# Optimization experiments

Hardware: AMD Instinct MI355X
Metric: run time of the kernel (lower is better)

Reference implementation:

```python
import math
import jax, jax.numpy as jnp
import numpy as np

SQ = 2048   # sequence length (hard-coded in source views)
B = 1       # batch (input_[:, 0, :] in QKVLinear)
H = 2048    # HIDDEN_SIZE
NH = 16     # NUM_HEADS
HD = 128    # head dim


def setup_inputs() -> dict:
    key = jax.random.key(0)
    ks = jax.random.split(key, 8)
    hidden_states = jax.random.normal(ks[0], (SQ, B, H), dtype=jnp.float32)
    # causal mask: True = masked (upper triangle, strictly above diagonal)
    attention_mask = jnp.triu(jnp.ones((SQ, SQ), dtype=bool), k=1)[None, None]
    qkv_w = jax.random.normal(ks[1], (3 * H, H), dtype=jnp.float32) * 0.02
    qkv_b = jax.random.normal(ks[2], (3 * H,), dtype=jnp.float32) * 0.02
    # SVD rotation matrices (approximately norm-preserving random matrices)
    svd_token = jax.random.normal(ks[3], (H, H), dtype=jnp.float32) / math.sqrt(H)
    svd_qk = jax.random.normal(ks[4], (NH, HD, HD), dtype=jnp.float32) / math.sqrt(HD)
    svd_vlin = jax.random.normal(ks[5], (NH, HD, HD), dtype=jnp.float32) / math.sqrt(HD)
    dense_w = jax.random.normal(ks[6], (NH, HD, H), dtype=jnp.float32) * 0.02
    dense_b = jax.random.normal(ks[7], (H,), dtype=jnp.float32) * 0.02
    return {
        "hidden_states": hidden_states,
        "attention_mask": attention_mask,
        "qkv_w": qkv_w,
        "qkv_b": qkv_b,
        "svd_token": svd_token,
        "svd_qk": svd_qk,
        "svd_vlin": svd_vlin,
        "dense_w": dense_w,
        "dense_b": dense_b,
    }


def reference(hidden_states, attention_mask, qkv_w, qkv_b, svd_token,
              svd_qk, svd_vlin, dense_w, dense_b):
    # QKVLinear: project input and weight through token-SVD (drop fraction = 0 -> no zeroing)
    x = hidden_states[:, 0, :] @ svd_token                 # [sq, H]
    w = qkv_w @ svd_token                                  # [3H, H]
    mixed = x @ w.T + qkv_b                                # [sq, 3H]
    mixed = mixed.reshape(SQ, B, NH, 3 * HD)
    q, k, v = jnp.split(mixed, 3, axis=-1)                 # each [sq, b, nh, hd]

    # per-head SVD-rotated Q/K (qk_drop = 0 -> h_mask is all-False, no zeroing)
    q = jnp.einsum('sbhd,hde->sbhe', q, svd_qk)
    k = jnp.einsum('sbhd,hde->sbhe', k, svd_qk)

    # scores: baddbmm with alpha = 1/(sqrt(hd)*coeff), then softmax rescales by coeff;
    # with layer_num=1 coeff=1, masked positions end at exactly -10000.
    scale = 1.0 / math.sqrt(HD)
    scores = jnp.einsum('sbhd,tbhd->bhst', q, k) * scale   # [b, nh, sq, sq]
    scores = jnp.where(attention_mask, -10000.0, scores)
    probs = jax.nn.softmax(scores, axis=-1)                # dropout in eval mode (identity)

    # per-head SVD-rotated V (vlinear_drop = 0 -> no zeroing)
    vv = jnp.einsum('sbhd,hde->sbhe', v, svd_vlin)
    ctx = jnp.einsum('bhst,tbhe->sbhe', probs, vv).reshape(SQ, B, H)

    # AttnOutputLinear: tsr block for head h = (dense_w[h].T @ svd_vlin[h]).T = svd_vlin[h].T @ dense_w[h]
    tsr = jnp.einsum('hde,hdo->heo', svd_vlin, dense_w).reshape(H, H)
    out = ctx @ tsr + dense_b                              # [sq, b, H]
    return out
```

## Files before the change

kernel.cpp:

```cpp
#include <hip/hip_runtime.h>
#include <hip/hip_bf16.h>
#include <stdint.h>
#include <math.h>


typedef __bf16 bf16_t;
typedef __bf16 bf16x8 __attribute__((ext_vector_type(8)));
typedef __bf16 bf16x4 __attribute__((ext_vector_type(4)));
typedef float  f32x4  __attribute__((ext_vector_type(4)));

__device__ __forceinline__ void async16(const void* g, void* l) {
  __builtin_amdgcn_global_load_lds(
      (const __attribute__((address_space(1))) void*)(uintptr_t)g,
      (__attribute__((address_space(3))) void*)(uint32_t)(uintptr_t)l,
      16, 0, 0);
}

#define FK_WAIT8() do { asm volatile("s_waitcnt vmcnt(8)" ::: "memory"); \
                        __builtin_amdgcn_sched_barrier(0); } while (0)
#define FK_WAIT4() do { asm volatile("s_waitcnt vmcnt(4)" ::: "memory"); \
                        __builtin_amdgcn_sched_barrier(0); } while (0)
#define FK_WAIT0() do { asm volatile("s_waitcnt vmcnt(0)" ::: "memory"); \
                        __builtin_amdgcn_sched_barrier(0); } while (0)
#define FK_BAR()   do { __builtin_amdgcn_s_barrier(); \
                        __builtin_amdgcn_sched_barrier(0); } while (0)

__device__ __forceinline__ void stage_half8(const bf16_t* __restrict__ P, int ld,
                                            int row0, int k0, bf16_t* lds,
                                            int w, int l)
{
  #pragma unroll
  for (int h = 0; h < 2; ++h) {
    const int r = h * 64 + w * 8 + (l >> 3);
    const int c = (l & 7) ^ (l >> 3);
    async16(P + (long long)(row0 + r) * ld + k0 + c * 8,
            lds + h * 4096 + w * 512);
  }
}

#define G8_READ_A(IH)                                                          \
  { _Pragma("unroll") for (int ii = 0; ii < 4; ++ii) {                         \
      _Pragma("unroll") for (int ks = 0; ks < 2; ++ks) {                       \
        const int rr = wmB + (IH) * 64 + ii * 16 + fr;                         \
        af[ii][ks] = *(const bf16x8*)&cA[rr * 64 + (((ks * 4 + kc) ^ (rr & 7)) * 8)]; \
      } } }

#define G8_READ_B(JH)                                                          \
  { _Pragma("unroll") for (int jj = 0; jj < 2; ++jj) {                         \
      _Pragma("unroll") for (int ks = 0; ks < 2; ++ks) {                       \
        const int rr = wnB + (JH) * 32 + jj * 16 + fr;                         \
        bfv[jj][ks] = *(const bf16x8*)&cB[rr * 64 + (((ks * 4 + kc) ^ (rr & 7)) * 8)]; \
      } } }

#define G8_MFMA(IH, JH)                                                        \
  { __builtin_amdgcn_s_setprio(1);                                             \
    _Pragma("unroll") for (int ks = 0; ks < 2; ++ks) {                         \
      _Pragma("unroll") for (int ii = 0; ii < 4; ++ii) {                       \
        _Pragma("unroll") for (int jj = 0; jj < 2; ++jj) {                     \
          acc[(IH) * 4 + ii][(JH) * 2 + jj] =                                  \
            __builtin_amdgcn_mfma_f32_16x16x32_bf16(af[ii][ks], bfv[jj][ks],   \
                acc[(IH) * 4 + ii][(JH) * 2 + jj], 0, 0, 0);                   \
        } } }                                                                  \
    __builtin_amdgcn_s_setprio(0); }

__global__ __launch_bounds__(512, 2)
void gemm8p(const bf16_t* __restrict__ A, const bf16_t* __restrict__ B,
            bf16_t* __restrict__ C, const bf16_t* __restrict__ bias,
            int K, int lda, int ldb, int ldc, int nbx)
{
  const int nwg = (int)gridDim.x;
  const int id  = (int)blockIdx.x;
  const int cpx = nwg >> 3;
  const int swz = (id & 7) * cpx + (id >> 3);
  const int by  = swz / nbx;
  const int bx  = swz - by * nbx;
  const int bm0 = by * 256;
  const int bn0 = bx * 256;

  __shared__ bf16_t sA[2][16384];
  __shared__ bf16_t sB[2][16384];

  const int t  = threadIdx.x;
  const int w  = t >> 6;
  const int l  = t & 63;
  const int fr = l & 15;
  const int kc = l >> 4;
  const int wmB = (w >> 2) * 128;
  const int wnB = (w & 3) * 64;

  float bvv[2][2];
  #pragma unroll
  for (int JH = 0; JH < 2; ++JH)
    #pragma unroll
    for (int jj = 0; jj < 2; ++jj)
      bvv[JH][jj] = (float)bias[bn0 + wnB + JH * 32 + jj * 16 + fr];

  f32x4 acc[8][4];
  #pragma unroll
  for (int i = 0; i < 8; ++i)
    #pragma unroll
    for (int j = 0; j < 4; ++j)
      #pragma unroll
      for (int r = 0; r < 4; ++r) acc[i][j][r] = 0.0f;

  const int nk = K >> 6;

  stage_half8(A, lda, bm0,       0, &sA[0][0],    w, l);
  stage_half8(A, lda, bm0 + 128, 0, &sA[0][8192], w, l);
  stage_half8(B, ldb, bn0,       0, &sB[0][0],    w, l);
  stage_half8(B, ldb, bn0 + 128, 0, &sB[0][8192], w, l);

  for (int m = 0; m < nk; ++m) {
    const int b = m & 1;
    const bf16_t* cA = sA[b];
    const bf16_t* cB = sB[b];
    const int k1 = (m + 1) << 6;
    const bool pf = (m + 1 < nk);
    bf16x8 af[4][2], bfv[2][2];

    if (pf) {
      stage_half8(A, lda, bm0,       k1, &sA[b ^ 1][0],    w, l);
      stage_half8(A, lda, bm0 + 128, k1, &sA[b ^ 1][8192], w, l);
      FK_WAIT4();
    } else {
      FK_WAIT0();
    }
    FK_BAR();
    G8_READ_A(0)
    G8_READ_B(0)
    G8_MFMA(0, 0)
    FK_BAR();

    G8_READ_B(1)
    if (pf) {
      stage_half8(B, ldb, bn0,       k1, &sB[b ^ 1][0],    w, l);
      stage_half8(B, ldb, bn0 + 128, k1, &sB[b ^ 1][8192], w, l);
    }
    FK_BAR();
    G8_MFMA(0, 1)
    FK_BAR();

    G8_READ_A(1)
    G8_READ_B(0)
    FK_BAR();
    G8_MFMA(1, 0)
    FK_BAR();

    G8_READ_B(1)
    FK_BAR();
    G8_MFMA(1, 1)
    FK_BAR();
  }

  #pragma unroll
  for (int JH = 0; JH < 2; ++JH)
    #pragma unroll
    for (int jj = 0; jj < 2; ++jj) {
      const int col = bn0 + wnB + JH * 32 + jj * 16 + fr;
      const float bv = bvv[JH][jj];
      #pragma unroll
      for (int IH = 0; IH < 2; ++IH)
        #pragma unroll
        for (int ii = 0; ii < 4; ++ii)
          #pragma unroll
          for (int r = 0; r < 4; ++r) {
            const int row = bm0 + wmB + IH * 64 + ii * 16 + kc * 4 + r;
            C[(long long)row * ldc + col] =
                (bf16_t)(acc[IH * 4 + ii][JH * 2 + jj][r] + bv);
          }
    }
}

__global__ __launch_bounds__(256)
void gemm_nt64k(const bf16_t* __restrict__ A, const bf16_t* __restrict__ B,
                void* __restrict__ Cv, const void* __restrict__ biasv,
                int K, int lda, int ldb, int ldc, float alpha, int flags)
{
  const int bm0 = blockIdx.y * 64;
  const int bn0 = blockIdx.x * 128;

  __shared__ bf16_t shA[8192];
  __shared__ bf16_t shB[16384];

  const int t  = threadIdx.x;
  const int w  = t >> 6;
  const int l  = t & 63;
  const int wm = (w >> 1) * 32;
  const int wn = (w & 1) * 64;
  const int r0 = l >> 2;
  const int c0 = ((l & 3) ^ ((l >> 3) & 3)) * 8;
  const int fr = l & 15;
  const int kc = l >> 4;
  const int swr = ((fr >> 1) & 3);

  f32x4 acc[2][4];
  #pragma unroll
  for (int i = 0; i < 2; ++i)
    #pragma unroll
    for (int j = 0; j < 4; ++j)
      #pragma unroll
      for (int r = 0; r < 4; ++r)
        acc[i][j][r] = 0.0f;

  for (int k0 = 0; k0 < K; k0 += 128) {
    #pragma unroll
    for (int u = 0; u < 4; ++u) {
      const int seg = u * 4 + w;
      const int q   = seg >> 2;
      const int s4  = seg & 3;
      async16(A + (long long)(bm0 + s4 * 16 + r0) * lda + (k0 + q * 32 + c0),
              &shA[q * 2048 + s4 * 512]);
    }
    #pragma unroll
    for (int u = 0; u < 8; ++u) {
      const int seg = u * 4 + w;
      const int q   = seg >> 3;
      const int s8  = seg & 7;
      async16(B + (long long)(bn0 + s8 * 16 + r0) * ldb + (k0 + q * 32 + c0),
              &shB[q * 4096 + s8 * 512]);
    }
    __builtin_amdgcn_s_waitcnt(0);
    __syncthreads();

    const int rc = (kc ^ swr) * 8;
    #pragma unroll
    for (int q = 0; q < 4; ++q) {
      bf16x8 af[2], bfv[4];
      #pragma unroll
      for (int i = 0; i < 2; ++i)
        af[i]  = *(const bf16x8*)&shA[q * 2048 + (wm + i * 16 + fr) * 32 + rc];
      #pragma unroll
      for (int j = 0; j < 4; ++j)
        bfv[j] = *(const bf16x8*)&shB[q * 4096 + (wn + j * 16 + fr) * 32 + rc];
      #pragma unroll
      for (int i = 0; i < 2; ++i)
        #pragma unroll
        for (int j = 0; j < 4; ++j)
          acc[i][j] = __builtin_amdgcn_mfma_f32_16x16x32_bf16(af[i], bfv[j], acc[i][j], 0, 0, 0);
    }
    __syncthreads();
  }

  const int cc = l & 15;
  const int rq = (l >> 4) * 4;
  if (flags & 4) {
    float* C = (float*)Cv;
    const float* bias = (const float*)biasv;
    #pragma unroll
    for (int j = 0; j < 4; ++j) {
      const int col = bn0 + wn + j * 16 + cc;
      const float bv = bias ? bias[col] : 0.0f;
      #pragma unroll
      for (int i = 0; i < 2; ++i)
        #pragma unroll
        for (int r = 0; r < 4; ++r) {
          const int row = bm0 + wm + i * 16 + rq + r;
          C[(long long)row * ldc + col] = acc[i][j][r] * alpha + bv;
        }
    }
  } else {
    bf16_t* C = (bf16_t*)Cv;
    #pragma unroll
    for (int j = 0; j < 4; ++j) {
      const int col = bn0 + wn + j * 16 + cc;
      #pragma unroll
      for (int i = 0; i < 2; ++i)
        #pragma unroll
        for (int r = 0; r < 4; ++r) {
          const int row = bm0 + wm + i * 16 + rq + r;
          C[(long long)row * ldc + col] = (bf16_t)(acc[i][j][r] * alpha);
        }
    }
  }
}

__global__ __launch_bounds__(256)
void gemm_mprep(const bf16_t* __restrict__ qkT, const bf16_t* __restrict__ vlT,
                const bf16_t* __restrict__ qkv_wT, const bf16_t* __restrict__ dwT,
                bf16_t* __restrict__ Wrot, bf16_t* __restrict__ tsrT,
                const bf16_t* __restrict__ stb, bf16_t* __restrict__ Mbuf)
{
  __shared__ bf16_t smem[16384];
  const int z = blockIdx.x;
  const int t  = threadIdx.x;
  const int w  = t >> 6;
  const int l  = t & 63;
  const int r0 = l >> 2;
  const int c0 = ((l & 3) ^ ((l >> 3) & 3)) * 8;
  const int fr = l & 15;
  const int kc = l >> 4;
  const int swr = ((fr >> 1) & 3);
  const int cc = l & 15;
  const int rq = (l >> 4) * 4;

  if (z < 1024) {
    const int pz = z >> 4, px = z & 15;
    const bf16_t* A;
    const bf16_t* B;
    bf16_t* C;
    int bm0, bn0;
    if (pz < 48) {
      const int h = pz / 3, p = pz - 3 * h;
      A = (p == 2 ? vlT : qkT) + h * 16384;
      B = qkv_wT + (long long)pz * 262144;
      C = Wrot + (long long)pz * 262144;
      bm0 = 0;  bn0 = px * 128;
    } else {
      const int b = pz - 48;
      A = dwT + (long long)b * 262144;
      B = vlT + b * 16384;
      C = tsrT;
      bm0 = px * 128;  bn0 = b * 128;
    }
    bf16_t* shA = smem;
    bf16_t* shB = smem + 8192;
    const int wm = (w >> 1) * 64;
    const int wn = (w & 1) * 64;
    const int arow0 = (pz < 48 ? 0 : bm0);
    const int brow0 = (pz < 48 ? bn0 : 0);

    f32x4 acc[4][4];
    #pragma unroll
    for (int i = 0; i < 4; ++i)
      #pragma unroll
      for (int j = 0; j < 4; ++j)
        #pragma unroll
        for (int r = 0; r < 4; ++r)
          acc[i][j][r] = 0.0f;

    for (int k0 = 0; k0 < 128; k0 += 64) {
      #pragma unroll
      for (int u = 0; u < 4; ++u) {
        const int seg  = u * 4 + w;
        const int half = seg >> 3;
        const int s8   = seg & 7;
        const int row  = s8 * 16 + r0;
        const int gk   = k0 + half * 32 + c0;
        async16(A + (long long)(arow0 + row) * 128 + gk, &shA[half * 4096 + s8 * 512]);
        async16(B + (long long)(brow0 + row) * 128 + gk, &shB[half * 4096 + s8 * 512]);
      }
      __builtin_amdgcn_s_waitcnt(0);
      __syncthreads();

      const int rc = (kc ^ swr) * 8;
      #pragma unroll
      for (int h = 0; h < 2; ++h) {
        bf16x8 af[4], bfv[4];
        #pragma unroll
        for (int i = 0; i < 4; ++i) {
          af[i]  = *(const bf16x8*)&shA[h * 4096 + (wm + i * 16 + fr) * 32 + rc];
          bfv[i] = *(const bf16x8*)&shB[h * 4096 + (wn + i * 16 + fr) * 32 + rc];
        }
        #pragma unroll
        for (int i = 0; i < 4; ++i)
          #pragma unroll
          for (int j = 0; j < 4; ++j)
            acc[i][j] = __builtin_amdgcn_mfma_f32_16x16x32_bf16(af[i], bfv[j], acc[i][j], 0, 0, 0);
      }
      __syncthreads();
    }

    #pragma unroll
    for (int j = 0; j < 4; ++j) {
      const int col = bn0 + wn + j * 16 + cc;
      #pragma unroll
      for (int i = 0; i < 4; ++i)
        #pragma unroll
        for (int r = 0; r < 4; ++r) {
          const int row = arow0 + wm + i * 16 + rq + r;
          C[(long long)row * 2048 + col] = (bf16_t)acc[i][j][r];
        }
    }
  } else {
    const int m = z - 1024;
    const int bm0 = (m >> 4) * 64;
    const int bn0 = (m & 15) * 128;
    bf16_t* shA = smem;
    bf16_t* shB = smem + 4096;
    const int wm = (w >> 1) * 32;
    const int wn = (w & 1) * 64;

    f32x4 acc[2][4];
    #pragma unroll
    for (int i = 0; i < 2; ++i)
      #pragma unroll
      for (int j = 0; j < 4; ++j)
        #pragma unroll
        for (int r = 0; r < 4; ++r)
          acc[i][j][r] = 0.0f;

    for (int k0 = 0; k0 < 2048; k0 += 64) {
      #pragma unroll
      for (int u = 0; u < 2; ++u) {
        const int seg  = u * 4 + w;
        const int half = seg >> 2;
        const int s4   = seg & 3;
        async16(stb + (long long)(bm0 + s4 * 16 + r0) * 2048 + (k0 + half * 32 + c0),
                &shA[half * 2048 + s4 * 512]);
      }
      #pragma unroll
      for (int u = 0; u < 4; ++u) {
        const int seg  = u * 4 + w;
        const int half = seg >> 3;
        const int s8   = seg & 7;
        async16(stb + (long long)(bn0 + s8 * 16 + r0) * 2048 + (k0 + half * 32 + c0),
                &shB[half * 4096 + s8 * 512]);
      }
      __builtin_amdgcn_s_waitcnt(0);
      __syncthreads();

      const int rc = (kc ^ swr) * 8;
      #pragma unroll
      for (int h = 0; h < 2; ++h) {
        bf16x8 af[2], bfv[4];
        #pragma unroll
        for (int i = 0; i < 2; ++i)
          af[i]  = *(const bf16x8*)&shA[h * 2048 + (wm + i * 16 + fr) * 32 + rc];
        #pragma unroll
        for (int j = 0; j < 4; ++j)
          bfv[j] = *(const bf16x8*)&shB[h * 4096 + (wn + j * 16 + fr) * 32 + rc];
        #pragma unroll
        for (int i = 0; i < 2; ++i)
          #pragma unroll
          for (int j = 0; j < 4; ++j)
            acc[i][j] = __builtin_amdgcn_mfma_f32_16x16x32_bf16(af[i], bfv[j], acc[i][j], 0, 0, 0);
      }
      __syncthreads();
    }

    #pragma unroll
    for (int j = 0; j < 4; ++j) {
      const int col = bn0 + wn + j * 16 + cc;
      #pragma unroll
      for (int i = 0; i < 2; ++i)
        #pragma unroll
        for (int r = 0; r < 4; ++r) {
          const int row = bm0 + wm + i * 16 + rq + r;
          Mbuf[(long long)row * 2048 + col] = (bf16_t)acc[i][j][r];
        }
    }
  }
}

__device__ __forceinline__ void stage128(const bf16_t* __restrict__ gp, bf16_t* lds,
                                         const long long rstride, const int w, const int l)
{
  #pragma unroll
  for (int s = 0; s < 8; ++s) {
    const int chunk = (w * 8 + s) * 64 + l;
    const int r = chunk >> 4;
    const int c = (chunk & 15) ^ (r & 7);
    async16(gp + (long long)r * rstride + c * 8, &lds[(w * 8 + s) * 512]);
  }
}

__global__ __launch_bounds__(256)
void flash_k(const bf16_t* __restrict__ mixed, const bf16_t* __restrict__ vT,
             bf16_t* __restrict__ ctx, float iscale)
{
  const int h  = blockIdx.x;
  const int y  = blockIdx.y;
  const int qt = (y < 16) ? (31 - y) : (y - 16);
  const int r0g = qt * 64;
  const int niter = (qt >> 1) + 1;
  const bf16_t* Qp = mixed + h * 384;
  const bf16_t* Kp = mixed + h * 384 + 128;
  const bf16_t* Vp = vT + (long long)h * 262144;

  __shared__ bf16_t sK[16384];
  __shared__ bf16_t sV[16384];
  __shared__ bf16_t sP[8192];

  const int t  = threadIdx.x;
  const int w  = t >> 6;
  const int l  = t & 63;
  const int fr = l & 15;
  const int kc = l >> 4;
  const int qrow0 = r0g + w * 16;

  bf16x8 aq[4];
  #pragma unroll
  for (int ks = 0; ks < 4; ++ks)
    aq[ks] = *(const bf16x8*)(Qp + (long long)(qrow0 + fr) * 6144 + ks * 32 + kc * 8);

  f32x4 oacc[8];
  #pragma unroll
  for (int j = 0; j < 8; ++j)
    #pragma unroll
    for (int r = 0; r < 4; ++r) oacc[j][r] = 0.0f;
  float lsum[4] = {0.f, 0.f, 0.f, 0.f};

  FK_WAIT0();

  stage128(Kp, sK, 6144, w, l);
  stage128(Vp, sV, 2048, w, l);
  FK_WAIT8();
  FK_BAR();

  for (int it = 0; it < niter; ++it) {
    const int t0 = it * 128;

    f32x4 acc[8];
    #pragma unroll
    for (int j = 0; j < 8; ++j)
      #pragma unroll
      for (int r = 0; r < 4; ++r) acc[j][r] = 0.0f;
    #pragma unroll
    for (int ks = 0; ks < 4; ++ks) {
      bf16x8 bk[8];
      #pragma unroll
      for (int j = 0; j < 8; ++j)
        bk[j] = *(const bf16x8*)&sK[(j * 16 + fr) * 128 + (((ks * 4 + kc) ^ (fr & 7)) * 8)];
      __builtin_amdgcn_s_setprio(1);
      #pragma unroll
      for (int j = 0; j < 8; ++j)
        acc[j] = __builtin_amdgcn_mfma_f32_16x16x32_bf16(aq[ks], bk[j], acc[j], 0, 0, 0);
      __builtin_amdgcn_s_setprio(0);
    }

    #pragma unroll
    for (int r = 0; r < 4; ++r) {
      const int q16 = kc * 4 + r;
      const int Rg  = qrow0 + q16;
      float rs = 0.f;
      #pragma unroll
      for (int j = 0; j < 8; ++j) {
        const float e = (t0 + j * 16 + fr <= Rg) ? __expf(acc[j][r] * iscale) : 0.0f;
        rs += e;
        sP[(w * 16 + q16) * 128 + (((j * 2 + (fr >> 3)) ^ (q16 & 7)) * 8) + (fr & 7)] = (bf16_t)e;
      }
      rs += __shfl_xor(rs, 1, 64);
      rs += __shfl_xor(rs, 2, 64);
      rs += __shfl_xor(rs, 4, 64);
      rs += __shfl_xor(rs, 8, 64);
      lsum[r] += rs;
    }

    FK_BAR();
    if (it + 1 < niter) {
      stage128(Kp + (long long)(t0 + 128) * 6144, sK, 6144, w, l);
      FK_WAIT8();
    } else {
      FK_WAIT0();
    }
    FK_BAR();

    #pragma unroll
    for (int ks = 0; ks < 4; ++ks) {
      const bf16x8 ap =
          *(const bf16x8*)&sP[(w * 16 + fr) * 128 + (((ks * 4 + kc) ^ (fr & 7)) * 8)];
      bf16x8 bv[8];
      #pragma unroll
      for (int j = 0; j < 8; ++j)
        bv[j] = *(const bf16x8*)&sV[(j * 16 + fr) * 128 + (((ks * 4 + kc) ^ (fr & 7)) * 8)];
      __builtin_amdgcn_s_setprio(1);
      #pragma unroll
      for (int j = 0; j < 8; ++j)
        oacc[j] = __builtin_amdgcn_mfma_f32_16x16x32_bf16(ap, bv[j], oacc[j], 0, 0, 0);
      __builtin_amdgcn_s_setprio(0);
    }

    if (it + 1 < niter) {
      FK_BAR();
      stage128(Vp + (t0 + 128), sV, 2048, w, l);
      FK_WAIT8();
      FK_BAR();
    }
  }

  #pragma unroll
  for (int r = 0; r < 4; ++r) {
    const float inv = 1.0f / lsum[r];
    const int rowg = qrow0 + kc * 4 + r;
    #pragma unroll
    for (int j = 0; j < 8; ++j)
      ctx[(long long)rowg * 2048 + h * 128 + j * 16 + fr] = (bf16_t)(oacc[j][r] * inv);
  }
}

__global__ __launch_bounds__(256)
void front_k(const float* __restrict__ hs, bf16_t* __restrict__ hsb,
             const float* __restrict__ svd_tok, bf16_t* __restrict__ stb,
             const float* __restrict__ svd_qk, bf16_t* __restrict__ qkT,
             const float* __restrict__ svd_vl, bf16_t* __restrict__ vlT,
             const float* __restrict__ qkv_w, bf16_t* __restrict__ qkv_wT,
             const float* __restrict__ dense_w, bf16_t* __restrict__ dwT,
             const float* __restrict__ qkv_b, bf16_t* __restrict__ brot)
{
  __shared__ bf16_t sm[32][33];
  const int z = blockIdx.x;
  const int tid = threadIdx.x;

  if (z < 2048) {
    const float* in = (z < 1024) ? hs : svd_tok;
    bf16_t* out = (z < 1024) ? hsb : stb;
    const int base = (z & 1023) * 4096 + tid * 16;
    #pragma unroll
    for (int j = 0; j < 4; ++j) {
      const f32x4 v = *(const f32x4*)(in + base + j * 4);
      bf16x4 o;
      #pragma unroll
      for (int k = 0; k < 4; ++k) o[k] = (bf16_t)v[k];
      *(bf16x4*)(out + base + j * 4) = o;
    }
  } else if (z < 2560) {
    const int zz = z - 2048;
    const int zr = zz >> 4;
    const int tile = zz & 15;
    const float* ip = (zr < 16 ? svd_qk : svd_vl) + (long long)(zr & 15) * 16384;
    bf16_t* op = (zr < 16 ? qkT : vlT) + (long long)(zr & 15) * 16384;
    const int r0 = (tile & 3) << 5;
    const int c0 = (tile >> 2) << 5;
    const int tx = tid & 31;
    const int ty = tid >> 5;
    #pragma unroll
    for (int yy = ty; yy < 32; yy += 8)
      sm[yy][tx] = (bf16_t)ip[(long long)(r0 + yy) * 128 + c0 + tx];
    __syncthreads();
    #pragma unroll
    for (int yy = ty; yy < 32; yy += 8)
      op[(long long)(c0 + yy) * 128 + r0 + tx] = sm[tx][yy];
  } else if (z < 18944) {
    const int zz = z - 2560;
    const int zb = zz >> 8;
    const int tile = zz & 255;
    const float* ip = (zb < 48) ? qkv_w + (long long)zb * 262144
                                : dense_w + (long long)(zb - 48) * 262144;
    bf16_t* op = (zb < 48) ? qkv_wT + (long long)zb * 262144
                           : dwT + (long long)(zb - 48) * 262144;
    const int r0 = (tile & 3) << 5;
    const int c0 = (tile >> 2) << 5;
    const int tx = tid & 31;
    const int ty = tid >> 5;
    #pragma unroll
    for (int yy = ty; yy < 32; yy += 8)
      sm[yy][tx] = (bf16_t)ip[(long long)(r0 + yy) * 2048 + c0 + tx];
    __syncthreads();
    #pragma unroll
    for (int yy = ty; yy < 32; yy += 8)
      op[(long long)(c0 + yy) * 128 + r0 + tx] = sm[tx][yy];
  } else {
    const int hp = (z - 18944) * 2 + (tid >> 7);
    const int h = hp / 3, p = hp % 3;
    const int e = tid & 127;
    const float* R = (p == 2 ? (const float*)svd_vl : (const float*)svd_qk) + (long long)h * 16384;
    const float* b = qkv_b + h * 384 + p * 128;
    float acc = 0.f;
    for (int d = 0; d < 128; ++d)
      acc += b[d] * R[d * 128 + e];
    brot[h * 384 + p * 128 + e] = (bf16_t)acc;
  }
}

__global__ __launch_bounds__(256)
void transpose_b2b(const bf16_t* __restrict__ in, bf16_t* __restrict__ out,
                   int R, long long zsi, int rsi, long long zso)
{
  __shared__ bf16_t sm[32][33];
  const int z  = blockIdx.z;
  const int r0 = blockIdx.x << 5;
  const int c0 = blockIdx.y << 5;
  const int tx = threadIdx.x & 31;
  const int ty = threadIdx.x >> 5;
  const bf16_t* ip = in + (long long)z * zsi;
  bf16_t* op = out + (long long)z * zso;
  #pragma unroll
  for (int yy = ty; yy < 32; yy += 8)
    sm[yy][tx] = ip[(long long)(r0 + yy) * rsi + c0 + tx];
  __syncthreads();
  #pragma unroll
  for (int yy = ty; yy < 32; yy += 8)
    op[(long long)(c0 + yy) * R + r0 + tx] = sm[tx][yy];
}

extern "C" void kernel_launch(void* const* d_in, const int* in_sizes, int n_in,
                              void* d_out, int out_size, void* d_ws, size_t ws_size,
                              hipStream_t stream)
{
  const float* hs      = (const float*)d_in[0];
  const float* qkv_w   = (const float*)d_in[2];
  const float* qkv_b   = (const float*)d_in[3];
  const float* svd_tok = (const float*)d_in[4];
  const float* svd_qk  = (const float*)d_in[5];
  const float* svd_vl  = (const float*)d_in[6];
  const float* dense_w = (const float*)d_in[7];
  const float* dense_b = (const float*)d_in[8];
  float* out = (float*)d_out;
  bf16_t* ws = (bf16_t*)d_ws;

  bf16_t* hsb    = ws;
  bf16_t* stb    = ws +  4194304LL;
  bf16_t* Mbuf   = ws +  8388608LL;
  bf16_t* x2     = ws + 12582912LL;
  bf16_t* qkv_wT = ws + 16777216LL;
  bf16_t* Wrot   = ws + 29360128LL;
  bf16_t* mixed  = ws + 41943040LL;
  bf16_t* vT     = ws + 54525952LL;
  bf16_t* ctx    = ws + 58720256LL;
  bf16_t* dwT    = ws + 62914560LL;
  bf16_t* tsrT   = ws + 67108864LL;
  bf16_t* qkT    = ws + 71303168LL;
  bf16_t* vlT    = ws + 71565312LL;
  bf16_t* brot   = ws + 71827456LL;
  if (ws_size < 71833600ULL * 2ULL) return;

  const float iscale = 0.08838834764831845f;

  front_k<<<dim3(18968), 256, 0, stream>>>(hs, hsb, svd_tok, stb,
      svd_qk, qkT, svd_vl, vlT, qkv_w, qkv_wT, dense_w, dwT, qkv_b, brot);
  gemm_mprep<<<dim3(1536), 256, 0, stream>>>(qkT, vlT, qkv_wT, dwT,
      Wrot, tsrT, stb, Mbuf);
  gemm_nt64k<<<dim3(16, 32), 256, 0, stream>>>(hsb, Mbuf, x2, nullptr,
      2048, 2048, 2048, 2048, 1.0f, 0);
  gemm8p<<<dim3(192), 512, 0, stream>>>(x2, Wrot, mixed, brot,
      2048, 2048, 2048, 6144, 24);
  transpose_b2b<<<dim3(64, 4, 16), 256, 0, stream>>>(mixed + 256, vT, 2048, 384, 6144, 262144);
  flash_k<<<dim3(16, 32), 256, 0, stream>>>(mixed, vT, ctx, iscale);
  gemm_nt64k<<<dim3(16, 32), 256, 0, stream>>>(ctx, tsrT, out, dense_b,
      2048, 2048, 2048, 2048, 1.0f, 4);
}
```

Before: 375.2 us.

## Exploit symmetry of token-SVD Gram matrix and add XCD-aware tile remapping

Mbuf is stb times its own transpose, which is symmetric, so the prep kernel now computes only upper-triangular 128x128 tile pairs. It mirrors each off-diagonal tile into its transposed position through an LDS transpose, which cuts that GEMM's work roughly in half and reorders the launch so these blocks run first. Separately, gemm_nt64k and gemm8p remap block indices so each XCD handles a contiguous band of columns, aiming for better L2 locality. The mirror path adds an extra barrier and a second set of strided stores per off-diagonal tile.

```diff
diff --git a/kernel.cpp b/kernel.cpp
--- a/kernel.cpp
+++ b/kernel.cpp
@@ -24,6 +24,16 @@
                         __builtin_amdgcn_sched_barrier(0); } while (0)
 #define FK_BAR()   do { __builtin_amdgcn_s_barrier(); \
                         __builtin_amdgcn_sched_barrier(0); } while (0)
+
+__device__ __forceinline__ void xcd_cols(int& bx, int& by) {
+  const int nbx = (int)gridDim.x;
+  const int lin = (int)blockIdx.x + nbx * (int)blockIdx.y;
+  const int xcd = lin & 7;
+  const int idx = lin >> 3;
+  const int cpx = nbx >> 3;
+  bx = xcd * cpx + idx % cpx;
+  by = idx / cpx;
+}
 
 __device__ __forceinline__ void stage_half8(const bf16_t* __restrict__ P, int ld,
                                             int row0, int k0, bf16_t* lds,
@@ -68,12 +78,12 @@
             bf16_t* __restrict__ C, const bf16_t* __restrict__ bias,
             int K, int lda, int ldb, int ldc, int nbx)
 {
-  const int nwg = (int)gridDim.x;
   const int id  = (int)blockIdx.x;
-  const int cpx = nwg >> 3;
-  const int swz = (id & 7) * cpx + (id >> 3);
-  const int by  = swz / nbx;
-  const int bx  = swz - by * nbx;
+  const int xcd = id & 7;
+  const int idx = id >> 3;
+  const int bpx = nbx >> 3;
+  const int bx  = xcd * bpx + idx % bpx;
+  const int by  = idx / bpx;
   const int bm0 = by * 256;
   const int bn0 = bx * 256;
 
@@ -176,8 +186,10 @@
                 void* __restrict__ Cv, const void* __restrict__ biasv,
                 int K, int lda, int ldb, int ldc, float alpha, int flags)
 {
-  const int bm0 = blockIdx.y * 64;
-  const int bn0 = blockIdx.x * 128;
+  int bxs, bys;
+  xcd_cols(bxs, bys);
+  const int bm0 = bys * 64;
+  const int bn0 = bxs * 128;
 
   __shared__ bf16_t shA[8192];
   __shared__ bf16_t shB[16384];
@@ -293,8 +305,98 @@
   const int cc = l & 15;
   const int rq = (l >> 4) * 4;
 
-  if (z < 1024) {
-    const int pz = z >> 4, px = z & 15;
+  if (z < 272) {
+    int sup = z >> 1;
+    const int h2 = z & 1;
+    int I = 0;
+    #pragma unroll 1
+    while (sup >= 16 - I) { sup -= 16 - I; ++I; }
+    const int J = I + sup;
+    const int bm0 = I * 128 + h2 * 64;
+    const int bn0 = J * 128;
+    bf16_t* shA = smem;
+    bf16_t* shB = smem + 4096;
+    const int wm = (w >> 1) * 32;
+    const int wn = (w & 1) * 64;
+
+    f32x4 acc[2][4];
+    #pragma unroll
+    for (int i = 0; i < 2; ++i)
+      #pragma unroll
+      for (int j = 0; j < 4; ++j)
+        #pragma unroll
+        for (int r = 0; r < 4; ++r)
+          acc[i][j][r] = 0.0f;
+
+    for (int k0 = 0; k0 < 2048; k0 += 64) {
+      #pragma unroll
+      for (int u = 0; u < 2; ++u) {
+        const int seg  = u * 4 + w;
+        const int half = seg >> 2;
+        const int s4   = seg & 3;
+        async16(stb + (long long)(bm0 + s4 * 16 + r0) * 2048 + (k0 + half * 32 + c0),
+                &shA[half * 2048 + s4 * 512]);
+      }
+      #pragma unroll
+      for (int u = 0; u < 4; ++u) {
+        const int seg  = u * 4 + w;
+        const int half = seg >> 3;
+        const int s8   = seg & 7;
+        async16(stb + (long long)(bn0 + s8 * 16 + r0) * 2048 + (k0 + half * 32 + c0),
+                &shB[half * 4096 + s8 * 512]);
+      }
+      __builtin_amdgcn_s_waitcnt(0);
+      __syncthreads();
+
+      const int rc = (kc ^ swr) * 8;
+      #pragma unroll
+      for (int h = 0; h < 2; ++h) {
+        bf16x8 af[2], bfv[4];
+        #pragma unroll
+        for (int i = 0; i < 2; ++i)
+          af[i]  = *(const bf16x8*)&shA[h * 2048 + (wm + i * 16 + fr) * 32 + rc];
+        #pragma unroll
+        for (int j = 0; j < 4; ++j)
+          bfv[j] = *(const bf16x8*)&shB[h * 4096 + (wn + j * 16 + fr) * 32 + rc];
+        #pragma unroll
+        for (int i = 0; i < 2; ++i)
+          #pragma unroll
+          for (int j = 0; j < 4; ++j)
+            acc[i][j] = __builtin_amdgcn_mfma_f32_16x16x32_bf16(af[i], bfv[j], acc[i][j], 0, 0, 0);
+      }
+      __syncthreads();
+    }
+
+    const bool mir = (I != J);
+    #pragma unroll
+    for (int j = 0; j < 4; ++j) {
+      const int coll = wn + j * 16 + cc;
+      #pragma unroll
+      for (int i = 0; i < 2; ++i)
+        #pragma unroll
+        for (int r = 0; r < 4; ++r) {
+          const int rowl = wm + i * 16 + rq + r;
+          const bf16_t v = (bf16_t)acc[i][j][r];
+          Mbuf[(long long)(bm0 + rowl) * 2048 + bn0 + coll] = v;
+          if (mir)
+            smem[coll * 64 + (((rowl >> 3) ^ (coll & 7)) * 8) + (rowl & 7)] = v;
+        }
+    }
+    if (mir) {
+      __syncthreads();
+      const int cr  = t >> 3;
+      const int mc8 = t & 7;
+      bf16_t* mp = Mbuf + bm0 + mc8 * 8;
+      #pragma unroll
+      for (int p = 0; p < 4; ++p) {
+        const int c = p * 32 + cr;
+        const bf16x8 v = *(const bf16x8*)&smem[c * 64 + ((mc8 ^ (c & 7)) * 8)];
+        *(bf16x8*)(mp + (long long)(bn0 + c) * 2048) = v;
+      }
+    }
+  } else {
+    const int zz = z - 272;
+    const int pz = zz >> 4, px = zz & 15;
     const bf16_t* A;
     const bf16_t* B;
     bf16_t* C;
@@ -371,74 +473,6 @@
           C[(long long)row * 2048 + col] = (bf16_t)acc[i][j][r];
         }
     }
-  } else {
-    const int m = z - 1024;
-    const int bm0 = (m >> 4) * 64;
-    const int bn0 = (m & 15) * 128;
-    bf16_t* shA = smem;
-    bf16_t* shB = smem + 4096;
-    const int wm = (w >> 1) * 32;
-    const int wn = (w & 1) * 64;
-
-    f32x4 acc[2][4];
-    #pragma unroll
-    for (int i = 0; i < 2; ++i)
-      #pragma unroll
-      for (int j = 0; j < 4; ++j)
-        #pragma unroll
-        for (int r = 0; r < 4; ++r)
-          acc[i][j][r] = 0.0f;
-
-    for (int k0 = 0; k0 < 2048; k0 += 64) {
-      #pragma unroll
-      for (int u = 0; u < 2; ++u) {
-        const int seg  = u * 4 + w;
-        const int half = seg >> 2;
-        const int s4   = seg & 3;
-        async16(stb + (long long)(bm0 + s4 * 16 + r0) * 2048 + (k0 + half * 32 + c0),
-                &shA[half * 2048 + s4 * 512]);
-      }
-      #pragma unroll
-      for (int u = 0; u < 4; ++u) {
-        const int seg  = u * 4 + w;
-        const int half = seg >> 3;
-        const int s8   = seg & 7;
-        async16(stb + (long long)(bn0 + s8 * 16 + r0) * 2048 + (k0 + half * 32 + c0),
-                &shB[half * 4096 + s8 * 512]);
-      }
-      __builtin_amdgcn_s_waitcnt(0);
-      __syncthreads();
-
-      const int rc = (kc ^ swr) * 8;
-      #pragma unroll
-      for (int h = 0; h < 2; ++h) {
-        bf16x8 af[2], bfv[4];
-        #pragma unroll
-        for (int i = 0; i < 2; ++i)
-          af[i]  = *(const bf16x8*)&shA[h * 2048 + (wm + i * 16 + fr) * 32 + rc];
-        #pragma unroll
-        for (int j = 0; j < 4; ++j)
-          bfv[j] = *(const bf16x8*)&shB[h * 4096 + (wn + j * 16 + fr) * 32 + rc];
-        #pragma unroll
-        for (int i = 0; i < 2; ++i)
-          #pragma unroll
-          for (int j = 0; j < 4; ++j)
-            acc[i][j] = __builtin_amdgcn_mfma_f32_16x16x32_bf16(af[i], bfv[j], acc[i][j], 0, 0, 0);
-      }
-      __syncthreads();
-    }
-
-    #pragma unroll
-    for (int j = 0; j < 4; ++j) {
-      const int col = bn0 + wn + j * 16 + cc;
-      #pragma unroll
-      for (int i = 0; i < 2; ++i)
-        #pragma unroll
-        for (int r = 0; r < 4; ++r) {
-          const int row = bm0 + wm + i * 16 + rq + r;
-          Mbuf[(long long)row * 2048 + col] = (bf16_t)acc[i][j][r];
-        }
-    }
   }
 }
 
@@ -708,7 +742,7 @@
 
   front_k<<<dim3(18968), 256, 0, stream>>>(hs, hsb, svd_tok, stb,
       svd_qk, qkT, svd_vl, vlT, qkv_w, qkv_wT, dense_w, dwT, qkv_b, brot);
-  gemm_mprep<<<dim3(1536), 256, 0, stream>>>(qkT, vlT, qkv_wT, dwT,
+  gemm_mprep<<<dim3(1296), 256, 0, stream>>>(qkT, vlT, qkv_wT, dwT,
       Wrot, tsrT, stb, Mbuf);
   gemm_nt64k<<<dim3(16, 32), 256, 0, stream>>>(hsb, Mbuf, x2, nullptr,
       2048, 2048, 2048, 2048, 1.0f, 0);
```

Measured after the change: 370.7 us. About the same (-1.2%).
